# Performance work log

Hardware: AMD Instinct MI355X
Metric: run time of the kernel (lower is better)

The kernel has to match this reference:

```python
import jax, jax.numpy as jnp
import numpy as np

HEADS = 8
DIM_HEAD = 64
QUERY_DIM = 512
CONTEXT_DIM = 512
OUT_DIM = 512
INNER = HEADS * DIM_HEAD  # 512


def setup_inputs() -> dict:
    key = jax.random.key(0)
    ks = jax.random.split(key, 6)
    B, N, S, M = 2, 1024, 4, 2048
    x = jax.random.normal(ks[0], (B, N, S, QUERY_DIM), dtype=jnp.float32)
    context = jax.random.normal(ks[1], (B, M, CONTEXT_DIM), dtype=jnp.float32)
    # Linear weights stored as [in, out] so y = x @ W (matches torch Linear with W.T)
    Wq = jax.random.normal(ks[2], (QUERY_DIM, INNER), dtype=jnp.float32) / np.sqrt(QUERY_DIM)
    Wkv = jax.random.normal(ks[3], (CONTEXT_DIM, 2 * INNER), dtype=jnp.float32) / np.sqrt(CONTEXT_DIM)
    Wo = jax.random.normal(ks[4], (INNER, OUT_DIM), dtype=jnp.float32) / np.sqrt(INNER)
    bo = jax.random.normal(ks[5], (OUT_DIM,), dtype=jnp.float32) * 0.01
    return {"x": x, "context": context, "Wq": Wq, "Wkv": Wkv, "Wo": Wo, "bo": bo}


def reference(x, context, Wq, Wkv, Wo, bo):
    B, N, S, _ = x.shape
    M = context.shape[1]
    scale = DIM_HEAD ** -0.5
    # projections
    q = (x @ Wq).reshape(B, N, S, HEADS, DIM_HEAD)            # b n s h d
    kv = context @ Wkv                                        # b m (2*inner)
    k, v = jnp.split(kv, 2, axis=-1)
    k = k.reshape(B, M, HEADS, DIM_HEAD)                      # b m h d
    v = v.reshape(B, M, HEADS, DIM_HEAD)
    # attention scores: [(b h) s n m] expressed as bhsnm
    sim = jnp.einsum('bnshd,bmhd->bhsnm', q, k) * scale
    attn = jax.nn.softmax(sim, axis=-1)
    out = jnp.einsum('bhsnm,bmhd->bnshd', attn, v)            # b n s h d
    out = out.reshape(B, N, S, INNER)
    return out @ Wo + bo
```

## Files before the change

### kernel.cpp

```cpp
#include <hip/hip_runtime.h>

typedef __bf16 bf16;
typedef __bf16 bf16x8 __attribute__((ext_vector_type(8)));
typedef __bf16 bf16x4 __attribute__((ext_vector_type(4)));
typedef float f32x4 __attribute__((ext_vector_type(4)));

#define SCL 0.18033688011112042f

__global__ __launch_bounds__(256) void prep_kernel(const float* __restrict__ x,
                                                   const float* __restrict__ ctx,
                                                   const float* __restrict__ Wq,
                                                   const float* __restrict__ Wkv,
                                                   const float* __restrict__ Wo,
                                                   bf16* __restrict__ xb,
                                                   bf16* __restrict__ cb,
                                                   bf16* __restrict__ Wqt,
                                                   bf16* __restrict__ Wkvt,
                                                   bf16* __restrict__ Wot) {
  const int bid = blockIdx.x;
  const int tid = threadIdx.x;
  if (bid < 3072) {
    const float* src;
    bf16* dst;
    size_t off;
    if (bid < 2048) { src = x; dst = xb; off = (size_t)bid * 2048; }
    else            { src = ctx; dst = cb; off = (size_t)(bid - 2048) * 2048; }
    size_t i = off + (size_t)tid * 8;
    float4 a0 = *(const float4*)&src[i];
    float4 a1 = *(const float4*)&src[i + 4];
    bf16x8 o;
    o[0] = (bf16)a0.x; o[1] = (bf16)a0.y; o[2] = (bf16)a0.z; o[3] = (bf16)a0.w;
    o[4] = (bf16)a1.x; o[5] = (bf16)a1.y; o[6] = (bf16)a1.z; o[7] = (bf16)a1.w;
    *(bf16x8*)&dst[i] = o;
  } else {
    __shared__ float tile[32][33];
    const int idx = bid - 3072;
    const int bx = idx & 63;
    const int k0 = (idx >> 6) * 32;
    const float* W; bf16* Wt; int N, n0;
    if (bx < 16)      { W = Wq;  Wt = Wqt;  N = 512;  n0 = bx * 32; }
    else if (bx < 48) { W = Wkv; Wt = Wkvt; N = 1024; n0 = (bx - 16) * 32; }
    else              { W = Wo;  Wt = Wot;  N = 512;  n0 = (bx - 48) * 32; }
    const int j = tid & 31, i0 = tid >> 5;
#pragma unroll
    for (int ii = 0; ii < 4; ii++) {
      int i = i0 * 4 + ii;
      tile[i][j] = W[(size_t)(k0 + i) * N + n0 + j];
    }
    __syncthreads();
#pragma unroll
    for (int ii = 0; ii < 4; ii++) {
      int i = i0 * 4 + ii;
      Wt[(size_t)(n0 + i) * 512 + k0 + j] = (bf16)tile[j][i];
    }
  }
}

__device__ __forceinline__ void gemm_db_core(const bf16* __restrict__ A,
                                             const bf16* __restrict__ Bt,
                                             int m0, int n0,
                                             bf16* As, bf16* Bs,
                                             f32x4 (&acc)[4][2],
                                             int wave, int lane, int tid) {
  const int l15 = lane & 15, quad = lane >> 4;
  const int psw = l15 & 7;
  const int wm = (wave >> 1) * 64, wn = (wave & 1) * 32;

  const int srow = tid >> 2, c0 = tid & 3;
  const int ssw = srow & 7;
  const int off0 = srow * 64 + ((c0 * 2) ^ ssw) * 8;
  const int off1 = srow * 64 + ((c0 * 2 + 1) ^ ssw) * 8;

  const bf16* Ag0 = A + (size_t)(m0 + srow) * 512 + c0 * 16;
  const bf16* Ag1 = A + (size_t)(m0 + 64 + srow) * 512 + c0 * 16;
  const bf16* Bg  = Bt + (size_t)(n0 + srow) * 512 + c0 * 16;

  uint4 a00 = *(const uint4*)Ag0, a01 = *(const uint4*)(Ag0 + 8);
  uint4 a10 = *(const uint4*)Ag1, a11 = *(const uint4*)(Ag1 + 8);
  uint4 b0  = *(const uint4*)Bg,  b1  = *(const uint4*)(Bg + 8);
  *(uint4*)&As[off0] = a00;            *(uint4*)&As[off1] = a01;
  *(uint4*)&As[64 * 64 + off0] = a10;  *(uint4*)&As[64 * 64 + off1] = a11;
  *(uint4*)&Bs[off0] = b0;             *(uint4*)&Bs[off1] = b1;

  for (int it = 0; it < 8; ++it) {
    __syncthreads();
    if (it < 7) {
      const int kt = (it + 1) * 64;
      a00 = *(const uint4*)(Ag0 + kt); a01 = *(const uint4*)(Ag0 + kt + 8);
      a10 = *(const uint4*)(Ag1 + kt); a11 = *(const uint4*)(Ag1 + kt + 8);
      b0  = *(const uint4*)(Bg + kt);  b1  = *(const uint4*)(Bg + kt + 8);
    }
    const bf16* Ac = As + (it & 1) * (128 * 64);
    const bf16* Bc = Bs + (it & 1) * (64 * 64);
#pragma unroll
    for (int h = 0; h < 2; h++) {
      bf16x8 af[4], bfr[2];
#pragma unroll
      for (int i = 0; i < 4; i++)
        af[i] = *(const bf16x8*)&Ac[(wm + i * 16 + l15) * 64 + (((h * 4 + quad) ^ psw) * 8)];
#pragma unroll
      for (int j = 0; j < 2; j++)
        bfr[j] = *(const bf16x8*)&Bc[(wn + j * 16 + l15) * 64 + (((h * 4 + quad) ^ psw) * 8)];
#pragma unroll
      for (int i = 0; i < 4; i++)
#pragma unroll
        for (int j = 0; j < 2; j++)
          acc[i][j] = __builtin_amdgcn_mfma_f32_16x16x32_bf16(af[i], bfr[j], acc[i][j], 0, 0, 0);
    }
    if (it < 7) {
      bf16* An = As + ((it + 1) & 1) * (128 * 64);
      bf16* Bn = Bs + ((it + 1) & 1) * (64 * 64);
      *(uint4*)&An[off0] = a00;            *(uint4*)&An[off1] = a01;
      *(uint4*)&An[64 * 64 + off0] = a10;  *(uint4*)&An[64 * 64 + off1] = a11;
      *(uint4*)&Bn[off0] = b0;             *(uint4*)&Bn[off1] = b1;
    }
  }
}

__global__ __launch_bounds__(256, 2) void proj_kernel(const bf16* __restrict__ xb,
                                                      const bf16* __restrict__ cb,
                                                      const bf16* __restrict__ Wqt,
                                                      const bf16* __restrict__ Wkvt,
                                                      bf16* __restrict__ qb,
                                                      bf16* __restrict__ Kb,
                                                      bf16* __restrict__ Vtb) {
  __shared__ __align__(16) bf16 As[2 * 128 * 64];
  __shared__ __align__(16) bf16 Bs[2 * 64 * 64];
  const int tid = threadIdx.x;
  const int wave = tid >> 6, lane = tid & 63;
  const int quad = lane >> 4, l15 = lane & 15;
  const int bid = blockIdx.x;
  f32x4 acc[4][2] = {};
  const int wm = (wave >> 1) * 64, wn = (wave & 1) * 32;

  if (bid < 512) {
    const int m0 = (bid & 63) * 128, n0 = (bid >> 6) * 64;
    gemm_db_core(xb, Wqt, m0, n0, As, Bs, acc, wave, lane, tid);
#pragma unroll
    for (int i = 0; i < 4; i++) {
      const int rowb = m0 + wm + i * 16 + quad * 4;
#pragma unroll
      for (int j = 0; j < 2; j++) {
        const int col = n0 + wn + j * 16 + l15;
#pragma unroll
        for (int r = 0; r < 4; r++)
          qb[(size_t)(rowb + r) * 512 + col] = (bf16)(acc[i][j][r] * SCL);
      }
    }
  } else {
    const int idx = bid - 512;
    const int m0 = (idx & 31) * 128, n0 = (idx >> 5) * 64;
    gemm_db_core(cb, Wkvt, m0, n0, As, Bs, acc, wave, lane, tid);
#pragma unroll
    for (int i = 0; i < 4; i++) {
      const int rowb = m0 + wm + i * 16 + quad * 4;
#pragma unroll
      for (int j = 0; j < 2; j++) {
        const int col = n0 + wn + j * 16 + l15;
        if (col < 512) {
#pragma unroll
          for (int r = 0; r < 4; r++)
            Kb[(size_t)(rowb + r) * 512 + col] = (bf16)acc[i][j][r];
        } else {
          const int hh = (col - 512) >> 6, d = (col - 512) & 63;
          const int bb = rowb >> 11, mb = rowb & 2047;
          bf16x4 pk;
          pk[0] = (bf16)acc[i][j][0]; pk[1] = (bf16)acc[i][j][1];
          pk[2] = (bf16)acc[i][j][2]; pk[3] = (bf16)acc[i][j][3];
          *(bf16x4*)&Vtb[((size_t)(bb * 8 + hh) * 64 + d) * 2048 + mb] = pk;
        }
      }
    }
  }
}

__global__ __launch_bounds__(256, 2) void outproj_kernel(const bf16* __restrict__ attn,
                                                         const bf16* __restrict__ Wot,
                                                         float* __restrict__ out,
                                                         const float* __restrict__ bias) {
  __shared__ __align__(16) bf16 As[2 * 128 * 64];
  __shared__ __align__(16) bf16 Bs[2 * 64 * 64];
  const int tid = threadIdx.x;
  const int wave = tid >> 6, lane = tid & 63;
  const int quad = lane >> 4, l15 = lane & 15;
  const int bid = blockIdx.x;
  const int m0 = (bid & 63) * 128, n0 = (bid >> 6) * 64;
  f32x4 acc[4][2] = {};
  gemm_db_core(attn, Wot, m0, n0, As, Bs, acc, wave, lane, tid);
  const int wm = (wave >> 1) * 64, wn = (wave & 1) * 32;
#pragma unroll
  for (int i = 0; i < 4; i++) {
    const int rowb = m0 + wm + i * 16 + quad * 4;
#pragma unroll
    for (int j = 0; j < 2; j++) {
      const int col = n0 + wn + j * 16 + l15;
      const float bv = bias[col];
#pragma unroll
      for (int r = 0; r < 4; r++)
        out[(size_t)(rowb + r) * 512 + col] = acc[i][j][r] + bv;
    }
  }
}

__global__ __launch_bounds__(256, 2) void attn_kernel(const bf16* __restrict__ q,
                                                      const bf16* __restrict__ Kb,
                                                      const bf16* __restrict__ Vtb,
                                                      bf16* __restrict__ attn_out) {
  const int tid = threadIdx.x;
  const int wave = tid >> 6, lane = tid & 63;
  const int quad = lane >> 4, l15 = lane & 15;
  const int bid = blockIdx.x;
  const int g = bid & 15, inner = bid >> 4;
  const int b = g >> 3, h = g & 7;
  const int s = inner & 3, nt = inner >> 2;
  const int n0 = nt * 128;

  __shared__ __align__(16) bf16 Kl[2][64 * 64];
  __shared__ __align__(16) bf16 Vl[2][64 * 64];
  __shared__ __align__(16) bf16 Pl[4][32 * 64];
  bf16* Pw = &Pl[wave][0];

  size_t qoff[2];
  bf16x8 qf[2][2];
#pragma unroll
  for (int cg = 0; cg < 2; cg++) {
    const int n = n0 + wave * 32 + cg * 16 + l15;
    qoff[cg] = ((size_t)((b * 1024 + n) * 4 + s)) * 512 + h * 64;
    qf[cg][0] = *(const bf16x8*)&q[qoff[cg] + quad * 8];
    qf[cg][1] = *(const bf16x8*)&q[qoff[cg] + 32 + quad * 8];
  }

  f32x4 o[2][4] = {};
  f32x4 ol[2] = {};
  bf16x8 ones;
#pragma unroll
  for (int i = 0; i < 8; i++) ones[i] = (bf16)1.0f;

  const int srow = tid >> 2, c0 = tid & 3;
  const bf16* Kg = Kb + (size_t)(b * 2048 + srow) * 512 + h * 64 + c0 * 16;
  const bf16* Vg = Vtb + ((size_t)(b * 8 + h) * 64 + srow) * 2048 + c0 * 16;
  const int ssw = srow & 7;
  const int koff0 = srow * 64 + ((c0 * 2) ^ ssw) * 8;
  const int koff1 = srow * 64 + ((c0 * 2 + 1) ^ ssw) * 8;

  uint4 kr0 = *(const uint4*)Kg;
  uint4 kr1 = *(const uint4*)(Kg + 8);
  uint4 vr0 = *(const uint4*)Vg;
  uint4 vr1 = *(const uint4*)(Vg + 8);
  *(uint4*)&Kl[0][koff0] = kr0; *(uint4*)&Kl[0][koff1] = kr1;
  *(uint4*)&Vl[0][koff0] = vr0; *(uint4*)&Vl[0][koff1] = vr1;

  const int psw = l15 & 7;

  for (int t = 0; t < 32; ++t) {
    __syncthreads();
    if (t < 31) {
      const bf16* kg = Kg + (size_t)(t + 1) * 64 * 512;
      const bf16* vg = Vg + (t + 1) * 64;
      kr0 = *(const uint4*)kg; kr1 = *(const uint4*)(kg + 8);
      vr0 = *(const uint4*)vg; vr1 = *(const uint4*)(vg + 8);
    }
    const bf16* Kc = &Kl[t & 1][0];
    const bf16* Vc = &Vl[t & 1][0];

    f32x4 sf[2][4];
#pragma unroll
    for (int mc = 0; mc < 4; mc++) {
      bf16x8 kf0 = *(const bf16x8*)&Kc[(mc * 16 + l15) * 64 + ((quad ^ psw) * 8)];
      bf16x8 kf1 = *(const bf16x8*)&Kc[(mc * 16 + l15) * 64 + (((4 + quad) ^ psw) * 8)];
#pragma unroll
      for (int cg = 0; cg < 2; cg++) {
        f32x4 z = {};
        z = __builtin_amdgcn_mfma_f32_16x16x32_bf16(kf0, qf[cg][0], z, 0, 0, 0);
        z = __builtin_amdgcn_mfma_f32_16x16x32_bf16(kf1, qf[cg][1], z, 0, 0, 0);
        sf[cg][mc] = z;
      }
    }

#pragma unroll
    for (int cg = 0; cg < 2; cg++)
#pragma unroll
      for (int mc = 0; mc < 4; mc++) {
        bf16x4 pk;
        pk[0] = (bf16)__builtin_amdgcn_exp2f(sf[cg][mc][0]);
        pk[1] = (bf16)__builtin_amdgcn_exp2f(sf[cg][mc][1]);
        pk[2] = (bf16)__builtin_amdgcn_exp2f(sf[cg][mc][2]);
        pk[3] = (bf16)__builtin_amdgcn_exp2f(sf[cg][mc][3]);
        *(bf16x4*)&Pw[(cg * 16 + l15) * 64 + (((mc * 2 + (quad >> 1)) ^ psw)) * 8 + (quad & 1) * 4] = pk;
      }

#pragma unroll
    for (int mch = 0; mch < 2; mch++) {
      bf16x8 pf[2];
#pragma unroll
      for (int cg = 0; cg < 2; cg++)
        pf[cg] = *(const bf16x8*)&Pw[(cg * 16 + l15) * 64 + (((mch * 4 + quad) ^ psw)) * 8];
#pragma unroll
      for (int dg = 0; dg < 4; dg++) {
        bf16x8 vf = *(const bf16x8*)&Vc[(dg * 16 + l15) * 64 + (((mch * 4 + quad) ^ psw)) * 8];
#pragma unroll
        for (int cg = 0; cg < 2; cg++)
          o[cg][dg] = __builtin_amdgcn_mfma_f32_16x16x32_bf16(vf, pf[cg], o[cg][dg], 0, 0, 0);
      }
#pragma unroll
      for (int cg = 0; cg < 2; cg++)
        ol[cg] = __builtin_amdgcn_mfma_f32_16x16x32_bf16(ones, pf[cg], ol[cg], 0, 0, 0);
    }

    if (t < 31) {
      bf16* Kn = &Kl[(t + 1) & 1][0];
      bf16* Vn = &Vl[(t + 1) & 1][0];
      *(uint4*)&Kn[koff0] = kr0; *(uint4*)&Kn[koff1] = kr1;
      *(uint4*)&Vn[koff0] = vr0; *(uint4*)&Vn[koff1] = vr1;
    }
  }

#pragma unroll
  for (int cg = 0; cg < 2; cg++) {
    const float inv = 1.0f / ol[cg][0];
#pragma unroll
    for (int dg = 0; dg < 4; dg++) {
      bf16x4 ok;
      ok[0] = (bf16)(o[cg][dg][0] * inv); ok[1] = (bf16)(o[cg][dg][1] * inv);
      ok[2] = (bf16)(o[cg][dg][2] * inv); ok[3] = (bf16)(o[cg][dg][3] * inv);
      *(bf16x4*)&attn_out[qoff[cg] + dg * 16 + quad * 4] = ok;
    }
  }
}

extern "C" void kernel_launch(void* const* d_in, const int* in_sizes, int n_in,
                              void* d_out, int out_size, void* d_ws, size_t ws_size,
                              hipStream_t stream) {
  const float* x = (const float*)d_in[0];
  const float* context = (const float*)d_in[1];
  const float* Wq = (const float*)d_in[2];
  const float* Wkv = (const float*)d_in[3];
  const float* Wo = (const float*)d_in[4];
  const float* bo = (const float*)d_in[5];
  float* out = (float*)d_out;

  char* ws = (char*)d_ws;
  bf16* xb   = (bf16*)(ws);
  bf16* cb   = (bf16*)(ws + (8u << 20));
  bf16* qb   = (bf16*)(ws + (12u << 20));
  bf16* Kb   = (bf16*)(ws + (20u << 20));
  bf16* Vtb  = (bf16*)(ws + (24u << 20));
  bf16* Wqt  = (bf16*)(ws + (28u << 20));
  bf16* Wkvt = (bf16*)(ws + (28u << 20) + 524288);
  bf16* Wot  = (bf16*)(ws + (28u << 20) + 1572864);
  bf16* attn = xb;

  prep_kernel<<<4096, 256, 0, stream>>>(x, context, Wq, Wkv, Wo, xb, cb, Wqt, Wkvt, Wot);
  proj_kernel<<<1024, 256, 0, stream>>>(xb, cb, Wqt, Wkvt, qb, Kb, Vtb);
  attn_kernel<<<512, 256, 0, stream>>>(qb, Kb, Vtb, attn);
  outproj_kernel<<<512, 256, 0, stream>>>(attn, Wot, out, bo);
}
```

Baseline: 156.2 us.

## Fuse fp32-to-bf16 input conversion into projection GEMM and stage V transpose in LDS

The projection kernel now loads fp32 x and context directly and converts them to bf16 while filling shared memory, which removes the separate conversion pass and its bf16 round trip through global memory. The prep kernel is reduced to a weight-transpose kernel. The V-output epilogue first writes the tile into LDS and then stores contiguous 16-byte rows of Vt, replacing scattered 8-byte stores. In exchange, each GEMM tile reads twice as many A bytes from global memory and uses more registers to hold the fp32 prefetch.

New measurement: 163.6 us. 4.7% more time.

```diff
diff --git a/kernel.cpp b/kernel.cpp
--- a/kernel.cpp
+++ b/kernel.cpp
@@ -7,56 +7,43 @@
 
 #define SCL 0.18033688011112042f
 
-__global__ __launch_bounds__(256) void prep_kernel(const float* __restrict__ x,
-                                                   const float* __restrict__ ctx,
-                                                   const float* __restrict__ Wq,
-                                                   const float* __restrict__ Wkv,
-                                                   const float* __restrict__ Wo,
-                                                   bf16* __restrict__ xb,
-                                                   bf16* __restrict__ cb,
-                                                   bf16* __restrict__ Wqt,
-                                                   bf16* __restrict__ Wkvt,
-                                                   bf16* __restrict__ Wot) {
-  const int bid = blockIdx.x;
+__device__ __forceinline__ uint4 pack8(float4 x, float4 y) {
+  bf16x8 r;
+  r[0] = (bf16)x.x; r[1] = (bf16)x.y; r[2] = (bf16)x.z; r[3] = (bf16)x.w;
+  r[4] = (bf16)y.x; r[5] = (bf16)y.y; r[6] = (bf16)y.z; r[7] = (bf16)y.w;
+  return *(uint4*)&r;
+}
+
+__global__ __launch_bounds__(256) void transpose_all(const float* __restrict__ Wq,
+                                                     const float* __restrict__ Wkv,
+                                                     const float* __restrict__ Wo,
+                                                     bf16* __restrict__ Wqt,
+                                                     bf16* __restrict__ Wkvt,
+                                                     bf16* __restrict__ Wot) {
+  __shared__ float tile[32][33];
+  const int bx = blockIdx.x;
+  const int k0 = blockIdx.y * 32;
+  const float* W; bf16* Wt; int N, n0;
+  if (bx < 16)      { W = Wq;  Wt = Wqt;  N = 512;  n0 = bx * 32; }
+  else if (bx < 48) { W = Wkv; Wt = Wkvt; N = 1024; n0 = (bx - 16) * 32; }
+  else              { W = Wo;  Wt = Wot;  N = 512;  n0 = (bx - 48) * 32; }
   const int tid = threadIdx.x;
-  if (bid < 3072) {
-    const float* src;
-    bf16* dst;
-    size_t off;
-    if (bid < 2048) { src = x; dst = xb; off = (size_t)bid * 2048; }
-    else            { src = ctx; dst = cb; off = (size_t)(bid - 2048) * 2048; }
-    size_t i = off + (size_t)tid * 8;
-    float4 a0 = *(const float4*)&src[i];
-    float4 a1 = *(const float4*)&src[i + 4];
-    bf16x8 o;
-    o[0] = (bf16)a0.x; o[1] = (bf16)a0.y; o[2] = (bf16)a0.z; o[3] = (bf16)a0.w;
-    o[4] = (bf16)a1.x; o[5] = (bf16)a1.y; o[6] = (bf16)a1.z; o[7] = (bf16)a1.w;
-    *(bf16x8*)&dst[i] = o;
-  } else {
-    __shared__ float tile[32][33];
-    const int idx = bid - 3072;
-    const int bx = idx & 63;
-    const int k0 = (idx >> 6) * 32;
-    const float* W; bf16* Wt; int N, n0;
-    if (bx < 16)      { W = Wq;  Wt = Wqt;  N = 512;  n0 = bx * 32; }
-    else if (bx < 48) { W = Wkv; Wt = Wkvt; N = 1024; n0 = (bx - 16) * 32; }
-    else              { W = Wo;  Wt = Wot;  N = 512;  n0 = (bx - 48) * 32; }
-    const int j = tid & 31, i0 = tid >> 5;
-#pragma unroll
-    for (int ii = 0; ii < 4; ii++) {
-      int i = i0 * 4 + ii;
-      tile[i][j] = W[(size_t)(k0 + i) * N + n0 + j];
-    }
-    __syncthreads();
-#pragma unroll
-    for (int ii = 0; ii < 4; ii++) {
-      int i = i0 * 4 + ii;
-      Wt[(size_t)(n0 + i) * 512 + k0 + j] = (bf16)tile[j][i];
-    }
-  }
-}
-
-__device__ __forceinline__ void gemm_db_core(const bf16* __restrict__ A,
+  const int j = tid & 31, i0 = tid >> 5;
+#pragma unroll
+  for (int ii = 0; ii < 4; ii++) {
+    int i = i0 * 4 + ii;
+    tile[i][j] = W[(size_t)(k0 + i) * N + n0 + j];
+  }
+  __syncthreads();
+#pragma unroll
+  for (int ii = 0; ii < 4; ii++) {
+    int i = i0 * 4 + ii;
+    Wt[(size_t)(n0 + i) * 512 + k0 + j] = (bf16)tile[j][i];
+  }
+}
+
+template <int AFP32, typename AT>
+__device__ __forceinline__ void gemm_db_core(const AT* __restrict__ A,
                                              const bf16* __restrict__ Bt,
                                              int m0, int n0,
                                              bf16* As, bf16* Bs,
@@ -71,24 +58,49 @@
   const int off0 = srow * 64 + ((c0 * 2) ^ ssw) * 8;
   const int off1 = srow * 64 + ((c0 * 2 + 1) ^ ssw) * 8;
 
-  const bf16* Ag0 = A + (size_t)(m0 + srow) * 512 + c0 * 16;
-  const bf16* Ag1 = A + (size_t)(m0 + 64 + srow) * 512 + c0 * 16;
-  const bf16* Bg  = Bt + (size_t)(n0 + srow) * 512 + c0 * 16;
-
-  uint4 a00 = *(const uint4*)Ag0, a01 = *(const uint4*)(Ag0 + 8);
-  uint4 a10 = *(const uint4*)Ag1, a11 = *(const uint4*)(Ag1 + 8);
-  uint4 b0  = *(const uint4*)Bg,  b1  = *(const uint4*)(Bg + 8);
-  *(uint4*)&As[off0] = a00;            *(uint4*)&As[off1] = a01;
-  *(uint4*)&As[64 * 64 + off0] = a10;  *(uint4*)&As[64 * 64 + off1] = a11;
-  *(uint4*)&Bs[off0] = b0;             *(uint4*)&Bs[off1] = b1;
+  const AT* Ag0 = A + (size_t)(m0 + srow) * 512 + c0 * 16;
+  const AT* Ag1 = A + (size_t)(m0 + 64 + srow) * 512 + c0 * 16;
+  const bf16* Bg = Bt + (size_t)(n0 + srow) * 512 + c0 * 16;
+
+  uint4 a00, a01, a10, a11, b0, b1;
+  float4 f[8];
+
+  if constexpr (AFP32) {
+    f[0] = *(const float4*)(Ag0);     f[1] = *(const float4*)(Ag0 + 4);
+    f[2] = *(const float4*)(Ag0 + 8); f[3] = *(const float4*)(Ag0 + 12);
+    f[4] = *(const float4*)(Ag1);     f[5] = *(const float4*)(Ag1 + 4);
+    f[6] = *(const float4*)(Ag1 + 8); f[7] = *(const float4*)(Ag1 + 12);
+  } else {
+    a00 = *(const uint4*)Ag0; a01 = *(const uint4*)(Ag0 + 8);
+    a10 = *(const uint4*)Ag1; a11 = *(const uint4*)(Ag1 + 8);
+  }
+  b0 = *(const uint4*)Bg; b1 = *(const uint4*)(Bg + 8);
+
+  if constexpr (AFP32) {
+    *(uint4*)&As[off0] = pack8(f[0], f[1]);
+    *(uint4*)&As[off1] = pack8(f[2], f[3]);
+    *(uint4*)&As[64 * 64 + off0] = pack8(f[4], f[5]);
+    *(uint4*)&As[64 * 64 + off1] = pack8(f[6], f[7]);
+  } else {
+    *(uint4*)&As[off0] = a00;            *(uint4*)&As[off1] = a01;
+    *(uint4*)&As[64 * 64 + off0] = a10;  *(uint4*)&As[64 * 64 + off1] = a11;
+  }
+  *(uint4*)&Bs[off0] = b0; *(uint4*)&Bs[off1] = b1;
 
   for (int it = 0; it < 8; ++it) {
     __syncthreads();
     if (it < 7) {
       const int kt = (it + 1) * 64;
-      a00 = *(const uint4*)(Ag0 + kt); a01 = *(const uint4*)(Ag0 + kt + 8);
-      a10 = *(const uint4*)(Ag1 + kt); a11 = *(const uint4*)(Ag1 + kt + 8);
-      b0  = *(const uint4*)(Bg + kt);  b1  = *(const uint4*)(Bg + kt + 8);
+      if constexpr (AFP32) {
+        f[0] = *(const float4*)(Ag0 + kt);      f[1] = *(const float4*)(Ag0 + kt + 4);
+        f[2] = *(const float4*)(Ag0 + kt + 8);  f[3] = *(const float4*)(Ag0 + kt + 12);
+        f[4] = *(const float4*)(Ag1 + kt);      f[5] = *(const float4*)(Ag1 + kt + 4);
+        f[6] = *(const float4*)(Ag1 + kt + 8);  f[7] = *(const float4*)(Ag1 + kt + 12);
+      } else {
+        a00 = *(const uint4*)(Ag0 + kt); a01 = *(const uint4*)(Ag0 + kt + 8);
+        a10 = *(const uint4*)(Ag1 + kt); a11 = *(const uint4*)(Ag1 + kt + 8);
+      }
+      b0 = *(const uint4*)(Bg + kt); b1 = *(const uint4*)(Bg + kt + 8);
     }
     const bf16* Ac = As + (it & 1) * (128 * 64);
     const bf16* Bc = Bs + (it & 1) * (64 * 64);
@@ -110,15 +122,22 @@
     if (it < 7) {
       bf16* An = As + ((it + 1) & 1) * (128 * 64);
       bf16* Bn = Bs + ((it + 1) & 1) * (64 * 64);
-      *(uint4*)&An[off0] = a00;            *(uint4*)&An[off1] = a01;
-      *(uint4*)&An[64 * 64 + off0] = a10;  *(uint4*)&An[64 * 64 + off1] = a11;
-      *(uint4*)&Bn[off0] = b0;             *(uint4*)&Bn[off1] = b1;
-    }
-  }
-}
-
-__global__ __launch_bounds__(256, 2) void proj_kernel(const bf16* __restrict__ xb,
-                                                      const bf16* __restrict__ cb,
+      if constexpr (AFP32) {
+        *(uint4*)&An[off0] = pack8(f[0], f[1]);
+        *(uint4*)&An[off1] = pack8(f[2], f[3]);
+        *(uint4*)&An[64 * 64 + off0] = pack8(f[4], f[5]);
+        *(uint4*)&An[64 * 64 + off1] = pack8(f[6], f[7]);
+      } else {
+        *(uint4*)&An[off0] = a00;            *(uint4*)&An[off1] = a01;
+        *(uint4*)&An[64 * 64 + off0] = a10;  *(uint4*)&An[64 * 64 + off1] = a11;
+      }
+      *(uint4*)&Bn[off0] = b0; *(uint4*)&Bn[off1] = b1;
+    }
+  }
+}
+
+__global__ __launch_bounds__(256, 2) void proj_kernel(const float* __restrict__ x,
+                                                      const float* __restrict__ ctx,
                                                       const bf16* __restrict__ Wqt,
                                                       const bf16* __restrict__ Wkvt,
                                                       bf16* __restrict__ qb,
@@ -135,7 +154,7 @@
 
   if (bid < 512) {
     const int m0 = (bid & 63) * 128, n0 = (bid >> 6) * 64;
-    gemm_db_core(xb, Wqt, m0, n0, As, Bs, acc, wave, lane, tid);
+    gemm_db_core<1>(x, Wqt, m0, n0, As, Bs, acc, wave, lane, tid);
 #pragma unroll
     for (int i = 0; i < 4; i++) {
       const int rowb = m0 + wm + i * 16 + quad * 4;
@@ -150,26 +169,48 @@
   } else {
     const int idx = bid - 512;
     const int m0 = (idx & 31) * 128, n0 = (idx >> 5) * 64;
-    gemm_db_core(cb, Wkvt, m0, n0, As, Bs, acc, wave, lane, tid);
-#pragma unroll
-    for (int i = 0; i < 4; i++) {
-      const int rowb = m0 + wm + i * 16 + quad * 4;
-#pragma unroll
-      for (int j = 0; j < 2; j++) {
-        const int col = n0 + wn + j * 16 + l15;
-        if (col < 512) {
+    gemm_db_core<1>(ctx, Wkvt, m0, n0, As, Bs, acc, wave, lane, tid);
+    if (n0 < 512) {
+#pragma unroll
+      for (int i = 0; i < 4; i++) {
+        const int rowb = m0 + wm + i * 16 + quad * 4;
+#pragma unroll
+        for (int j = 0; j < 2; j++) {
+          const int col = n0 + wn + j * 16 + l15;
 #pragma unroll
           for (int r = 0; r < 4; r++)
             Kb[(size_t)(rowb + r) * 512 + col] = (bf16)acc[i][j][r];
-        } else {
-          const int hh = (col - 512) >> 6, d = (col - 512) & 63;
-          const int bb = rowb >> 11, mb = rowb & 2047;
+        }
+      }
+    } else {
+      __syncthreads();
+      bf16* Vs = As;
+      const int h = (n0 - 512) >> 6;
+      const int bb = m0 >> 11, mbase = m0 & 2047;
+#pragma unroll
+      for (int i = 0; i < 4; i++) {
+        const int ml = wm + i * 16 + quad * 4;
+#pragma unroll
+        for (int j = 0; j < 2; j++) {
+          const int d = wn + j * 16 + l15;
           bf16x4 pk;
           pk[0] = (bf16)acc[i][j][0]; pk[1] = (bf16)acc[i][j][1];
           pk[2] = (bf16)acc[i][j][2]; pk[3] = (bf16)acc[i][j][3];
-          *(bf16x4*)&Vtb[((size_t)(bb * 8 + hh) * 64 + d) * 2048 + mb] = pk;
+          *(bf16x4*)&Vs[d * 136 + ml] = pk;
         }
       }
+      __syncthreads();
+      const int dd = tid >> 2, mc2 = tid & 3;
+      const bf16* src = &Vs[dd * 136 + mc2 * 32];
+      uint4 v0 = *(const uint4*)(src);
+      uint4 v1 = *(const uint4*)(src + 8);
+      uint4 v2 = *(const uint4*)(src + 16);
+      uint4 v3 = *(const uint4*)(src + 24);
+      bf16* dst = &Vtb[(((size_t)bb * 8 + h) * 64 + dd) * 2048 + mbase + mc2 * 32];
+      *(uint4*)(dst) = v0;
+      *(uint4*)(dst + 8) = v1;
+      *(uint4*)(dst + 16) = v2;
+      *(uint4*)(dst + 24) = v3;
     }
   }
 }
@@ -186,7 +227,7 @@
   const int bid = blockIdx.x;
   const int m0 = (bid & 63) * 128, n0 = (bid >> 6) * 64;
   f32x4 acc[4][2] = {};
-  gemm_db_core(attn, Wot, m0, n0, As, Bs, acc, wave, lane, tid);
+  gemm_db_core<0>(attn, Wot, m0, n0, As, Bs, acc, wave, lane, tid);
   const int wm = (wave >> 1) * 64, wn = (wave & 1) * 32;
 #pragma unroll
   for (int i = 0; i < 4; i++) {
@@ -340,18 +381,16 @@
   float* out = (float*)d_out;
 
   char* ws = (char*)d_ws;
-  bf16* xb   = (bf16*)(ws);
-  bf16* cb   = (bf16*)(ws + (8u << 20));
-  bf16* qb   = (bf16*)(ws + (12u << 20));
-  bf16* Kb   = (bf16*)(ws + (20u << 20));
-  bf16* Vtb  = (bf16*)(ws + (24u << 20));
-  bf16* Wqt  = (bf16*)(ws + (28u << 20));
-  bf16* Wkvt = (bf16*)(ws + (28u << 20) + 524288);
-  bf16* Wot  = (bf16*)(ws + (28u << 20) + 1572864);
-  bf16* attn = xb;
-
-  prep_kernel<<<4096, 256, 0, stream>>>(x, context, Wq, Wkv, Wo, xb, cb, Wqt, Wkvt, Wot);
-  proj_kernel<<<1024, 256, 0, stream>>>(xb, cb, Wqt, Wkvt, qb, Kb, Vtb);
+  bf16* attn = (bf16*)(ws);
+  bf16* qb   = (bf16*)(ws + (8u << 20));
+  bf16* Kb   = (bf16*)(ws + (16u << 20));
+  bf16* Vtb  = (bf16*)(ws + (20u << 20));
+  bf16* Wqt  = (bf16*)(ws + (24u << 20));
+  bf16* Wkvt = (bf16*)(ws + (24u << 20) + 524288);
+  bf16* Wot  = (bf16*)(ws + (24u << 20) + 1572864);
+
+  transpose_all<<<dim3(64, 16), 256, 0, stream>>>(Wq, Wkv, Wo, Wqt, Wkvt, Wot);
+  proj_kernel<<<1024, 256, 0, stream>>>(x, context, Wqt, Wkvt, qb, Kb, Vtb);
   attn_kernel<<<512, 256, 0, stream>>>(qb, Kb, Vtb, attn);
   outproj_kernel<<<512, 256, 0, stream>>>(attn, Wot, out, bo);
 }
```
